# Optimization experiments

Hardware: AMD Instinct MI355X
Metric: run time of the kernel (lower is better)

## Reference

```python
import jax, jax.numpy as jnp
import numpy as np

B, N_IN, N_OUT, N, L, T_SS = 256, 1024, 256, 2048, 4, 32


def setup_inputs() -> dict:
    key = jax.random.key(0)
    ks = jax.random.split(key, 7)
    s_in = 1.0 / np.sqrt(N_IN)
    s_rec = 1.0 / np.sqrt(N)
    return {
        "X": jax.random.normal(ks[0], (B, N_IN), jnp.float32),
        "W_in_w": jax.random.uniform(ks[1], (N, N_IN), jnp.float32, -s_in, s_in),
        "W_in_b": jax.random.uniform(ks[2], (N,), jnp.float32, -s_in, s_in),
        "W_rec_w": jax.random.uniform(ks[3], (L, N, N), jnp.float32, -s_rec, s_rec),
        "W_rec_b": jax.random.uniform(ks[4], (L, N), jnp.float32, -s_rec, s_rec),
        "W_out_w": jax.random.uniform(ks[5], (N_OUT, N), jnp.float32, -s_rec, s_rec),
        "W_out_b": jax.random.uniform(ks[6], (N_OUT,), jnp.float32, -s_rec, s_rec),
        "T": T_SS,
    }


def reference(X, W_in_w, W_in_b, W_rec_w, W_rec_b, W_out_w, W_out_b, T):
    x_in = X @ W_in_w.T + W_in_b  # (B, N)
    h0 = jnp.zeros((L, X.shape[0], N), X.dtype)

    def step(h, _):
        # layer 0 driven by input projection; layers l>0 driven by layer l-1
        new0 = jnp.sin(x_in + h[0] @ W_rec_w[0].T + W_rec_b[0])
        hs = [new0]
        for l in range(1, L):
            hs.append(jnp.sin(hs[-1] + h[l] @ W_rec_w[l].T + W_rec_b[l]))
        return jnp.stack(hs), None

    h_final, _ = jax.lax.scan(step, h0, None, length=T)
    return h_final[-1] @ W_out_w.T + W_out_b
```

## Files before the change

### kernel.cpp

```cpp
#include <hip/hip_runtime.h>

typedef unsigned short u16;
typedef unsigned char u8;
typedef unsigned int u32;
typedef __bf16 bf16x8 __attribute__((ext_vector_type(8)));
typedef float f32x4 __attribute__((ext_vector_type(4)));
typedef u32 u32x4 __attribute__((ext_vector_type(4)));
typedef u16 u16x4 __attribute__((ext_vector_type(4)));
typedef int i32x4 __attribute__((ext_vector_type(4)));

#define NH 2048
#define BATCH 256
#define NIN 1024
#define NOUT 256
#define LAY 4
#define TSS 32
#define BK 64

#define SW_W 5747.0f
#define INV_DQ (1.0f / (127.0f * 5747.0f))

#define WAITVM(N) asm volatile("s_waitcnt vmcnt(" #N ")" ::: "memory")

__device__ __forceinline__ u16 f2bf(float f) {
  u32 u = __builtin_bit_cast(u32, f);
  u = (u + 0x7FFFu + ((u >> 16) & 1u)) >> 16;
  return (u16)u;
}
__device__ __forceinline__ float bf2f(u16 h) {
  u32 u = ((u32)h) << 16;
  return __builtin_bit_cast(float, u);
}

__device__ __forceinline__ float fast_sin(float x) {
  float k = __builtin_rintf(x * 0.3183098861837907f);
  float r = __builtin_fmaf(k, -3.14159274101257324f, x);
  r = __builtin_fmaf(k, 8.742277657347586e-08f, r);
  float s = r * r;
  float p = __builtin_fmaf(s, 2.75573192e-06f, -1.98412698e-04f);
  p = __builtin_fmaf(s, p, 8.33333333e-03f);
  p = __builtin_fmaf(s, p, -1.66666667e-01f);
  p = r + r * s * p;
  int ki = (int)k;
  return (ki & 1) ? -p : p;
}

__device__ __forceinline__ bf16x8 ld_frag(const u16* p) {
  u32x4 r = *(const u32x4*)p;
  return __builtin_bit_cast(bf16x8, r);
}

__device__ __forceinline__ f32x4 mfma16(bf16x8 a, bf16x8 b, f32x4 c) {
  return __builtin_amdgcn_mfma_f32_16x16x32_bf16(a, b, c, 0, 0, 0);
}

__device__ __forceinline__ i32x4 mfma_i8(i32x4 a, i32x4 b, i32x4 c) {
  return __builtin_amdgcn_mfma_i32_16x16x64_i8(a, b, c, 0, 0, 0);
}

__device__ __forceinline__ void gload16(const void* g, void* lds) {
  __builtin_amdgcn_global_load_lds(
      (__attribute__((address_space(1))) u32*)g,
      (__attribute__((address_space(3))) u32*)lds, 16, 0, 0);
}


__global__ __launch_bounds__(256) void k_cvt_w8(const float* __restrict__ in,
                                                u32* __restrict__ out, int n4) {
  int i = blockIdx.x * 256 + threadIdx.x;
  if (i >= n4) return;
  f32x4 v = ((const f32x4*)in)[i];
  u32 o = 0;
  #pragma unroll
  for (int j = 0; j < 4; j++) {
    int q = (int)__builtin_rintf(v[j] * SW_W);
    o |= ((u32)(q & 255)) << (8 * j);
  }
  out[i] = o;
}

__global__ __launch_bounds__(256) void k_split2(const float* __restrict__ in,
                                                u16* __restrict__ hi,
                                                u16* __restrict__ lo, int n4) {
  int i = blockIdx.x * 256 + threadIdx.x;
  if (i >= n4) return;
  f32x4 v = ((const f32x4*)in)[i];
  u16x4 hv, lv;
  #pragma unroll
  for (int j = 0; j < 4; j++) {
    u16 h = f2bf(v[j]);
    hv[j] = h;
    lv[j] = f2bf(v[j] - bf2f(h));
  }
  ((u16x4*)hi)[i] = hv;
  ((u16x4*)lo)[i] = lv;
}


struct GemmArgs {
  const u16* A[4];
  const u16* B[4];
  void* G;
  int ldA, ldB, kiters, nl;
};

template <int OBF, int NKS>
__global__ __launch_bounds__(256, 2) void k_gemm(GemmArgs args) {
  __shared__ alignas(16) u16 Ab[2][128 * BK];
  __shared__ alignas(16) u16 Bb[2][128 * BK];

  int bid = blockIdx.x;
  int nl = args.nl;
  int l = bid % nl;
  int t1 = bid / nl;
  int ks = t1 & (NKS - 1);
  int t2 = t1 / NKS;
  int nt = t2 & 15;
  int mt = t2 >> 4;

  int tid = threadIdx.x;
  int w = tid >> 6, lane = tid & 63;
  int l15 = lane & 15, l4 = lane >> 4;
  int ldA = args.ldA, ldB = args.ldB;
  int kiters = args.kiters;

  const u16* Ag = args.A[l] + (size_t)(mt * 128) * ldA + ks * (kiters * BK);
  const u16* Bg = args.B[l] + (size_t)(nt * 128) * ldB + ks * (kiters * BK);

  int srow = w * 32 + (lane >> 3);
  int csrc = ((lane & 7) ^ (lane >> 3)) * 8;
  int agoff[4], bgoff[4], lbase[4];
  #pragma unroll
  for (int j = 0; j < 4; j++) {
    agoff[j] = (srow + j * 8) * ldA + csrc;
    bgoff[j] = (srow + j * 8) * ldB + csrc;
    lbase[j] = w * 2048 + j * 512;
  }

  int wr = w >> 1, wc = w & 1;

  f32x4 zero = {0.f, 0.f, 0.f, 0.f};
  f32x4 acc[4][4];
  #pragma unroll
  for (int m = 0; m < 4; m++)
    #pragma unroll
    for (int n = 0; n < 4; n++) acc[m][n] = zero;

  auto stage = [&](int bufi, int kb) {
    int k0 = kb * BK;
    #pragma unroll
    for (int j = 0; j < 4; j++) {
      gload16(Ag + agoff[j] + k0, &Ab[bufi][lbase[j]]);
      gload16(Bg + bgoff[j] + k0, &Bb[bufi][lbase[j]]);
    }
  };
  auto compute = [&](int bufi) {
    #pragma unroll
    for (int kk = 0; kk < 2; kk++) {
      int swz = ((kk * 4 + l4) ^ (l15 & 7)) * 8;
      bf16x8 a[4], b[4];
      #pragma unroll
      for (int m = 0; m < 4; m++)
        a[m] = ld_frag(&Ab[bufi][(wr * 64 + m * 16 + l15) * BK + swz]);
      #pragma unroll
      for (int n = 0; n < 4; n++)
        b[n] = ld_frag(&Bb[bufi][(wc * 64 + n * 16 + l15) * BK + swz]);
      #pragma unroll
      for (int m = 0; m < 4; m++)
        #pragma unroll
        for (int n = 0; n < 4; n++)
          acc[m][n] = mfma16(a[m], b[n], acc[m][n]);
    }
  };

  stage(0, 0);
  stage(1, 1);

  int cur = 0;
  for (int kb = 0; kb < kiters - 2; kb++) {
    WAITVM(8);
    __builtin_amdgcn_s_barrier();
    compute(cur);
    __builtin_amdgcn_s_barrier();
    stage(cur, kb + 2);
    cur ^= 1;
  }
  WAITVM(8);
  __builtin_amdgcn_s_barrier();
  compute(cur);
  cur ^= 1;
  WAITVM(0);
  __builtin_amdgcn_s_barrier();
  compute(cur);

  size_t obase = ((size_t)(ks * nl + l) * BATCH + mt * 128) * NH + nt * 128;
  if (OBF) {
    u16* Go = (u16*)args.G + obase;
    #pragma unroll
    for (int m = 0; m < 4; m++) {
      int row = wr * 64 + m * 16 + l4 * 4;
      #pragma unroll
      for (int n = 0; n < 4; n++) {
        int col = wc * 64 + n * 16 + l15;
        #pragma unroll
        for (int r = 0; r < 4; r++)
          Go[(size_t)(row + r) * NH + col] = f2bf(acc[m][n][r]);
      }
    }
  } else {
    float* Go = (float*)args.G + obase;
    #pragma unroll
    for (int m = 0; m < 4; m++) {
      int row = wr * 64 + m * 16 + l4 * 4;
      #pragma unroll
      for (int n = 0; n < 4; n++) {
        int col = wc * 64 + n * 16 + l15;
        #pragma unroll
        for (int r = 0; r < 4; r++)
          Go[(size_t)(row + r) * NH + col] = acc[m][n][r];
      }
    }
  }
}


struct Rec8Args {
  const u8* h;
  const u8* W8;
  u16* Gp;
};

__global__ __launch_bounds__(256, 2) void k_gemm8(Rec8Args args) {
  __shared__ alignas(16) u8 Ab[2][128 * 128];
  __shared__ alignas(16) u8 Bb[2][128 * 128];

  int bid = blockIdx.x;
  int l = bid & 3;
  int ks = (bid >> 2) & 3;
  int nt = (bid >> 4) & 15;
  int mt = bid >> 8;

  int tid = threadIdx.x;
  int lane = tid & 63;
  int w = tid >> 6;
  int l15 = lane & 15, l4 = lane >> 4;
  int wr = w >> 1, wc = w & 1;

  const u8* Ag = args.h + (size_t)l * (BATCH * NH) + (size_t)(mt * 128) * NH + ks * 512;
  const u8* Bg = args.W8 + (size_t)l * (NH * NH) + (size_t)(nt * 128) * NH + ks * 512;

  int srow = tid >> 3;
  int csrc = ((tid & 7) ^ (srow & 7)) * 16;
  int goff[4], lbase[4];
  #pragma unroll
  for (int j = 0; j < 4; j++) {
    goff[j] = (j * 32 + srow) * NH + csrc;
    lbase[j] = j * 4096 + tid * 16;
  }

  i32x4 zero = {0, 0, 0, 0};
  i32x4 acc[4][4];
  #pragma unroll
  for (int m = 0; m < 4; m++)
    #pragma unroll
    for (int n = 0; n < 4; n++) acc[m][n] = zero;

  auto stage = [&](int bufi, int kb) {
    int k0 = kb * 128;
    #pragma unroll
    for (int j = 0; j < 4; j++) {
      gload16(Ag + goff[j] + k0, &Ab[bufi][lbase[j]]);
      gload16(Bg + goff[j] + k0, &Bb[bufi][lbase[j]]);
    }
  };
  auto compute = [&](int bufi) {
    #pragma unroll
    for (int kk = 0; kk < 2; kk++) {
      int swz = ((kk * 4 + l4) ^ (l15 & 7)) * 16;
      i32x4 a[4], b[4];
      #pragma unroll
      for (int m = 0; m < 4; m++)
        a[m] = *(const i32x4*)&Ab[bufi][(wr * 64 + m * 16 + l15) * 128 + swz];
      #pragma unroll
      for (int n = 0; n < 4; n++)
        b[n] = *(const i32x4*)&Bb[bufi][(wc * 64 + n * 16 + l15) * 128 + swz];
      #pragma unroll
      for (int m = 0; m < 4; m++)
        #pragma unroll
        for (int n = 0; n < 4; n++)
          acc[m][n] = mfma_i8(a[m], b[n], acc[m][n]);
    }
  };

  stage(0, 0);
  stage(1, 1);

  int cur = 0;
  #pragma unroll 1
  for (int kb = 0; kb < 2; kb++) {
    WAITVM(8);
    __builtin_amdgcn_s_barrier();
    compute(cur);
    __builtin_amdgcn_s_barrier();
    stage(cur, kb + 2);
    cur ^= 1;
  }
  WAITVM(8);
  __builtin_amdgcn_s_barrier();
  compute(cur);
  cur ^= 1;
  WAITVM(0);
  __builtin_amdgcn_s_barrier();
  compute(cur);

  u16* Go = args.Gp + (size_t)(ks * LAY + l) * (BATCH * NH) +
            (size_t)(mt * 128) * NH + nt * 128;
  #pragma unroll
  for (int m = 0; m < 4; m++) {
    int row = wr * 64 + m * 16 + l4 * 4;
    #pragma unroll
    for (int n = 0; n < 4; n++) {
      int col = wc * 64 + n * 16 + l15;
      #pragma unroll
      for (int r = 0; r < 4; r++)
        Go[(size_t)(row + r) * NH + col] = f2bf((float)acc[m][n][r] * INV_DQ);
    }
  }
}

__global__ __launch_bounds__(256) void k_chain8(const u16* __restrict__ Gp,
                                                const float* __restrict__ x_in,
                                                const float* __restrict__ brec,
                                                u8* __restrict__ hq,
                                                u16* __restrict__ h3bf) {
  int i = blockIdx.x * 256 + threadIdx.x;
  int e = i * 4;
  int col = e & (NH - 1);
  f32x4 pre = *(const f32x4*)(x_in + e);
  #pragma unroll
  for (int l = 0; l < LAY; l++) {
    u16x4 g0 = *(const u16x4*)(Gp + (size_t)(0 * LAY + l) * (BATCH * NH) + e);
    u16x4 g1 = *(const u16x4*)(Gp + (size_t)(1 * LAY + l) * (BATCH * NH) + e);
    u16x4 g2 = *(const u16x4*)(Gp + (size_t)(2 * LAY + l) * (BATCH * NH) + e);
    u16x4 g3 = *(const u16x4*)(Gp + (size_t)(3 * LAY + l) * (BATCH * NH) + e);
    f32x4 bb = *(const f32x4*)(brec + l * NH + col);
    u32 qw = 0;
    u16x4 hv;
    #pragma unroll
    for (int j = 0; j < 4; j++) {
      float v = fast_sin(pre[j] + (bf2f(g0[j]) + bf2f(g1[j])) +
                         (bf2f(g2[j]) + bf2f(g3[j])) + bb[j]);
      pre[j] = v;
      int q = (int)__builtin_rintf(v * 127.0f);
      qw |= ((u32)(q & 255)) << (8 * j);
      hv[j] = f2bf(v);
    }
    *(u32*)(hq + (size_t)l * (BATCH * NH) + e) = qw;
    if (l == LAY - 1) *(u16x4*)(h3bf + e) = hv;
  }
}

__global__ __launch_bounds__(256) void k_xin_fin(const float* __restrict__ Gp2,
                                                 const float* __restrict__ bin,
                                                 float* __restrict__ x_in) {
  int i = blockIdx.x * 256 + threadIdx.x;
  int e = i * 4;
  int col = e & (NH - 1);
  f32x4 s = *(const f32x4*)(bin + col);
  #pragma unroll
  for (int t = 0; t < 6; t++)
    s += *(const f32x4*)(Gp2 + (size_t)t * (BATCH * NH) + e);
  *(f32x4*)(x_in + e) = s;
}

__global__ __launch_bounds__(64) void k_gemm_out(const u16* __restrict__ h3,
                                                 const u16* __restrict__ Wh,
                                                 const u16* __restrict__ Wl,
                                                 const float* __restrict__ bout,
                                                 float* __restrict__ out) {
  int bid = blockIdx.x;
  int mt = bid & 7, nt = bid >> 3;
  int lane = threadIdx.x;
  int l15 = lane & 15, l4 = lane >> 4;
  f32x4 zero = {0.f, 0.f, 0.f, 0.f};
  f32x4 acc0 = zero, acc1 = zero;
  const u16* a0p = h3 + (size_t)(mt * 32 + l15) * NH + l4 * 8;
  const u16* a1p = a0p + 16 * NH;
  const u16* bhp = Wh + (size_t)(nt * 16 + l15) * NH + l4 * 8;
  const u16* blp = Wl + (size_t)(nt * 16 + l15) * NH + l4 * 8;
  for (int kb = 0; kb < 64; kb++) {
    bf16x8 a0 = ld_frag(a0p + kb * 32);
    bf16x8 a1 = ld_frag(a1p + kb * 32);
    bf16x8 bh = ld_frag(bhp + kb * 32);
    bf16x8 bl = ld_frag(blp + kb * 32);
    acc0 = mfma16(a0, bh, acc0);
    acc0 = mfma16(a0, bl, acc0);
    acc1 = mfma16(a1, bh, acc1);
    acc1 = mfma16(a1, bl, acc1);
  }
  float bo = bout[nt * 16 + l15];
  #pragma unroll
  for (int r = 0; r < 4; r++) {
    out[(size_t)(mt * 32 + l4 * 4 + r) * NOUT + nt * 16 + l15] = acc0[r] + bo;
    out[(size_t)(mt * 32 + 16 + l4 * 4 + r) * NOUT + nt * 16 + l15] = acc1[r] + bo;
  }
}


extern "C" void kernel_launch(void* const* d_in, const int* in_sizes, int n_in,
                              void* d_out, int out_size, void* d_ws, size_t ws_size,
                              hipStream_t stream) {
  const float* X     = (const float*)d_in[0];
  const float* Winw  = (const float*)d_in[1];
  const float* Winb  = (const float*)d_in[2];
  const float* Wrw   = (const float*)d_in[3];
  const float* Wrb   = (const float*)d_in[4];
  const float* Woutw = (const float*)d_in[5];
  const float* Woutb = (const float*)d_in[6];
  float* out = (float*)d_out;

  char* ws = (char*)d_ws;
  u8*  W8     = (u8*)(ws);
  u8*  h0i    = (u8*)(ws + 16777216);
  u8*  h1i    = (u8*)(ws + 18874368);
  u16* h3bf   = (u16*)(ws + 20971520);
  float* xin  = (float*)(ws + 22020096);
  u16* Gp     = (u16*)(ws + 24117248);
  float* Gp2  = (float*)(ws + 40894464);
  u16* Xhi    = (u16*)(ws + 53477376);
  u16* Xlo    = (u16*)(ws + 54001664);
  u16* Winh   = (u16*)(ws + 54525952);
  u16* Winl   = (u16*)(ws + 58720256);
  u16* Wouth  = (u16*)(ws + 62914560);
  u16* Woutl  = (u16*)(ws + 63963136);

  k_cvt_w8<<<16384, 256, 0, stream>>>(Wrw, (u32*)W8, 4194304);
  k_split2<<<256, 256, 0, stream>>>(X, Xhi, Xlo, 65536);
  k_split2<<<2048, 256, 0, stream>>>(Winw, Winh, Winl, 524288);
  k_split2<<<512, 256, 0, stream>>>(Woutw, Wouth, Woutl, 131072);
  hipMemsetAsync(h0i, 0, 2097152, stream);

  GemmArgs ax;
  ax.A[0] = Xhi; ax.A[1] = Xhi; ax.A[2] = Xlo; ax.A[3] = Xhi;
  ax.B[0] = Winh; ax.B[1] = Winl; ax.B[2] = Winh; ax.B[3] = Winh;
  ax.G = Gp2; ax.ldA = NIN; ax.ldB = NIN; ax.kiters = 8; ax.nl = 3;
  k_gemm<0, 2><<<192, 256, 0, stream>>>(ax);
  k_xin_fin<<<512, 256, 0, stream>>>(Gp2, Winb, xin);

  u8* hin = h0i;
  u8* hout = h1i;
  for (int t = 0; t < TSS; t++) {
    Rec8Args ar;
    ar.h = hin; ar.W8 = W8; ar.Gp = Gp;
    k_gemm8<<<512, 256, 0, stream>>>(ar);
    k_chain8<<<512, 256, 0, stream>>>(Gp, xin, Wrb, hout, h3bf);
    u8* tmp = hin; hin = hout; hout = tmp;
  }

  k_gemm_out<<<128, 64, 0, stream>>>(h3bf, Wouth, Woutl, Woutb, out);
}
```

Baseline: 662.1 us.

## Fuse recurrent int8 GEMM and sin chain into one per-step kernel

Each timestep's split-K int8 GEMM over the four layers and the separate sine-chain kernel are replaced by one kernel. Each block computes a 32x64 tile for all four layers over the full K range and applies bias, sine, quantization and the bf16 store in registers. This drops the bf16 partial-sum buffer round trip and one launch per step. The cost is far less work per block: a tiny tile with 2 MFMAs per layer per k-slice, only 256 blocks, occupancy 1, and byte-wide scattered output stores.

Measured after the change: 653.1 us. Within noise of the previous version (-1.4%).

```diff
diff --git a/kernel.cpp b/kernel.cpp
--- a/kernel.cpp
+++ b/kernel.cpp
@@ -224,71 +224,74 @@
 }
 
 
-struct Rec8Args {
-  const u8* h;
+struct StepArgs {
+  const u8* hin;
   const u8* W8;
-  u16* Gp;
+  u8* hout;
+  u16* h3bf;
+  const float* xin;
+  const float* brec;
 };
 
-__global__ __launch_bounds__(256, 2) void k_gemm8(Rec8Args args) {
-  __shared__ alignas(16) u8 Ab[2][128 * 128];
-  __shared__ alignas(16) u8 Bb[2][128 * 128];
+__global__ __launch_bounds__(256, 1) void k_step(StepArgs args) {
+  __shared__ alignas(16) u8 Ab[2][LAY][32 * 128];
+  __shared__ alignas(16) u8 Bb[2][LAY][64 * 128];
 
   int bid = blockIdx.x;
-  int l = bid & 3;
-  int ks = (bid >> 2) & 3;
-  int nt = (bid >> 4) & 15;
-  int mt = bid >> 8;
+  int nt8 = bid & 7;
+  int mt = (bid >> 3) & 7;
+  int ntl = bid >> 6;
+  int nt = nt8 * 4 + ntl;
 
   int tid = threadIdx.x;
   int lane = tid & 63;
   int w = tid >> 6;
   int l15 = lane & 15, l4 = lane >> 4;
-  int wr = w >> 1, wc = w & 1;
-
-  const u8* Ag = args.h + (size_t)l * (BATCH * NH) + (size_t)(mt * 128) * NH + ks * 512;
-  const u8* Bg = args.W8 + (size_t)l * (NH * NH) + (size_t)(nt * 128) * NH + ks * 512;
+  int wr = w & 1, wc = w >> 1;
 
   int srow = tid >> 3;
   int csrc = ((tid & 7) ^ (srow & 7)) * 16;
-  int goff[4], lbase[4];
-  #pragma unroll
-  for (int j = 0; j < 4; j++) {
-    goff[j] = (j * 32 + srow) * NH + csrc;
-    lbase[j] = j * 4096 + tid * 16;
+
+  const u8* Ag[LAY];
+  const u8* Bg[LAY];
+  #pragma unroll
+  for (int l = 0; l < LAY; l++) {
+    Ag[l] = args.hin + (size_t)l * (BATCH * NH) + (size_t)(mt * 32) * NH;
+    Bg[l] = args.W8 + (size_t)l * (NH * NH) + (size_t)(nt * 64) * NH;
   }
 
   i32x4 zero = {0, 0, 0, 0};
-  i32x4 acc[4][4];
-  #pragma unroll
-  for (int m = 0; m < 4; m++)
-    #pragma unroll
-    for (int n = 0; n < 4; n++) acc[m][n] = zero;
+  i32x4 acc[LAY][2];
+  #pragma unroll
+  for (int l = 0; l < LAY; l++) {
+    acc[l][0] = zero;
+    acc[l][1] = zero;
+  }
 
   auto stage = [&](int bufi, int kb) {
     int k0 = kb * 128;
     #pragma unroll
-    for (int j = 0; j < 4; j++) {
-      gload16(Ag + goff[j] + k0, &Ab[bufi][lbase[j]]);
-      gload16(Bg + goff[j] + k0, &Bb[bufi][lbase[j]]);
-    }
+    for (int l = 0; l < LAY; l++)
+      gload16(Ag[l] + srow * NH + csrc + k0, &Ab[bufi][l][tid * 16]);
+    #pragma unroll
+    for (int l = 0; l < LAY; l++)
+      #pragma unroll
+      for (int j = 0; j < 2; j++)
+        gload16(Bg[l] + (size_t)(j * 32 + srow) * NH + csrc + k0,
+                &Bb[bufi][l][j * 4096 + tid * 16]);
   };
   auto compute = [&](int bufi) {
     #pragma unroll
     for (int kk = 0; kk < 2; kk++) {
       int swz = ((kk * 4 + l4) ^ (l15 & 7)) * 16;
-      i32x4 a[4], b[4];
-      #pragma unroll
-      for (int m = 0; m < 4; m++)
-        a[m] = *(const i32x4*)&Ab[bufi][(wr * 64 + m * 16 + l15) * 128 + swz];
-      #pragma unroll
-      for (int n = 0; n < 4; n++)
-        b[n] = *(const i32x4*)&Bb[bufi][(wc * 64 + n * 16 + l15) * 128 + swz];
-      #pragma unroll
-      for (int m = 0; m < 4; m++)
-        #pragma unroll
-        for (int n = 0; n < 4; n++)
-          acc[m][n] = mfma_i8(a[m], b[n], acc[m][n]);
+      #pragma unroll
+      for (int l = 0; l < LAY; l++) {
+        i32x4 a = *(const i32x4*)&Ab[bufi][l][(wr * 16 + l15) * 128 + swz];
+        i32x4 b0 = *(const i32x4*)&Bb[bufi][l][(wc * 32 + l15) * 128 + swz];
+        i32x4 b1 = *(const i32x4*)&Bb[bufi][l][(wc * 32 + 16 + l15) * 128 + swz];
+        acc[l][0] = mfma_i8(a, b0, acc[l][0]);
+        acc[l][1] = mfma_i8(a, b1, acc[l][1]);
+      }
     }
   };
 
@@ -297,15 +300,15 @@
 
   int cur = 0;
   #pragma unroll 1
-  for (int kb = 0; kb < 2; kb++) {
-    WAITVM(8);
+  for (int kb = 0; kb < 14; kb++) {
+    WAITVM(12);
     __builtin_amdgcn_s_barrier();
     compute(cur);
     __builtin_amdgcn_s_barrier();
     stage(cur, kb + 2);
     cur ^= 1;
   }
-  WAITVM(8);
+  WAITVM(12);
   __builtin_amdgcn_s_barrier();
   compute(cur);
   cur ^= 1;
@@ -313,50 +316,27 @@
   __builtin_amdgcn_s_barrier();
   compute(cur);
 
-  u16* Go = args.Gp + (size_t)(ks * LAY + l) * (BATCH * NH) +
-            (size_t)(mt * 128) * NH + nt * 128;
-  #pragma unroll
-  for (int m = 0; m < 4; m++) {
-    int row = wr * 64 + m * 16 + l4 * 4;
-    #pragma unroll
-    for (int n = 0; n < 4; n++) {
-      int col = wc * 64 + n * 16 + l15;
-      #pragma unroll
-      for (int r = 0; r < 4; r++)
-        Go[(size_t)(row + r) * NH + col] = f2bf((float)acc[m][n][r] * INV_DQ);
-    }
-  }
-}
-
-__global__ __launch_bounds__(256) void k_chain8(const u16* __restrict__ Gp,
-                                                const float* __restrict__ x_in,
-                                                const float* __restrict__ brec,
-                                                u8* __restrict__ hq,
-                                                u16* __restrict__ h3bf) {
-  int i = blockIdx.x * 256 + threadIdx.x;
-  int e = i * 4;
-  int col = e & (NH - 1);
-  f32x4 pre = *(const f32x4*)(x_in + e);
-  #pragma unroll
-  for (int l = 0; l < LAY; l++) {
-    u16x4 g0 = *(const u16x4*)(Gp + (size_t)(0 * LAY + l) * (BATCH * NH) + e);
-    u16x4 g1 = *(const u16x4*)(Gp + (size_t)(1 * LAY + l) * (BATCH * NH) + e);
-    u16x4 g2 = *(const u16x4*)(Gp + (size_t)(2 * LAY + l) * (BATCH * NH) + e);
-    u16x4 g3 = *(const u16x4*)(Gp + (size_t)(3 * LAY + l) * (BATCH * NH) + e);
-    f32x4 bb = *(const f32x4*)(brec + l * NH + col);
-    u32 qw = 0;
-    u16x4 hv;
-    #pragma unroll
-    for (int j = 0; j < 4; j++) {
-      float v = fast_sin(pre[j] + (bf2f(g0[j]) + bf2f(g1[j])) +
-                         (bf2f(g2[j]) + bf2f(g3[j])) + bb[j]);
-      pre[j] = v;
-      int q = (int)__builtin_rintf(v * 127.0f);
-      qw |= ((u32)(q & 255)) << (8 * j);
-      hv[j] = f2bf(v);
-    }
-    *(u32*)(hq + (size_t)l * (BATCH * NH) + e) = qw;
-    if (l == LAY - 1) *(u16x4*)(h3bf + e) = hv;
+  #pragma unroll
+  for (int n = 0; n < 2; n++) {
+    int col = nt * 64 + wc * 32 + n * 16 + l15;
+    float bb[LAY];
+    #pragma unroll
+    for (int l = 0; l < LAY; l++) bb[l] = args.brec[l * NH + col];
+    #pragma unroll
+    for (int r = 0; r < 4; r++) {
+      int row = mt * 32 + wr * 16 + l4 * 4 + r;
+      size_t base = (size_t)row * NH + col;
+      float pre = args.xin[base];
+      #pragma unroll
+      for (int l = 0; l < LAY; l++) {
+        float g = (float)acc[l][n][r] * INV_DQ;
+        float v = fast_sin(pre + g + bb[l]);
+        pre = v;
+        int q = (int)__builtin_rintf(v * 127.0f);
+        args.hout[(size_t)l * (BATCH * NH) + base] = (u8)(q & 255);
+        if (l == LAY - 1) args.h3bf[base] = f2bf(v);
+      }
+    }
   }
 }
 
@@ -425,14 +405,13 @@
   u8*  h1i    = (u8*)(ws + 18874368);
   u16* h3bf   = (u16*)(ws + 20971520);
   float* xin  = (float*)(ws + 22020096);
-  u16* Gp     = (u16*)(ws + 24117248);
-  float* Gp2  = (float*)(ws + 40894464);
-  u16* Xhi    = (u16*)(ws + 53477376);
-  u16* Xlo    = (u16*)(ws + 54001664);
-  u16* Winh   = (u16*)(ws + 54525952);
-  u16* Winl   = (u16*)(ws + 58720256);
-  u16* Wouth  = (u16*)(ws + 62914560);
-  u16* Woutl  = (u16*)(ws + 63963136);
+  float* Gp2  = (float*)(ws + 24117248);
+  u16* Xhi    = (u16*)(ws + 36700160);
+  u16* Xlo    = (u16*)(ws + 37224448);
+  u16* Winh   = (u16*)(ws + 37748736);
+  u16* Winl   = (u16*)(ws + 41943040);
+  u16* Wouth  = (u16*)(ws + 46137344);
+  u16* Woutl  = (u16*)(ws + 47185920);
 
   k_cvt_w8<<<16384, 256, 0, stream>>>(Wrw, (u32*)W8, 4194304);
   k_split2<<<256, 256, 0, stream>>>(X, Xhi, Xlo, 65536);
@@ -450,10 +429,10 @@
   u8* hin = h0i;
   u8* hout = h1i;
   for (int t = 0; t < TSS; t++) {
-    Rec8Args ar;
-    ar.h = hin; ar.W8 = W8; ar.Gp = Gp;
-    k_gemm8<<<512, 256, 0, stream>>>(ar);
-    k_chain8<<<512, 256, 0, stream>>>(Gp, xin, Wrb, hout, h3bf);
+    StepArgs ar;
+    ar.hin = hin; ar.W8 = W8; ar.hout = hout; ar.h3bf = h3bf;
+    ar.xin = xin; ar.brec = Wrb;
+    k_step<<<256, 256, 0, stream>>>(ar);
     u8* tmp = hin; hin = hout; hout = tmp;
   }
 
```
